# Kernel optimization log

Measured on AMD Instinct MI355X. Metric: run time of the kernel, lower is better.

The kernel has to match this reference:

```python
import jax, jax.numpy as jnp
import numpy as np

N, E, B = 30000, 480000, 64
F_IN, HID, ED = 128, 64, 32
NEG, EPS = 0.2, 1e-5


def _add_self_loops(edge_index, edge_attr):
    # PyG add_self_loops with fill_value='mean': self-loop edge_attr of node i
    # is the mean of edge_attr over edges whose destination is i.
    src, dst = edge_index[0], edge_index[1]
    cnt = jax.ops.segment_sum(jnp.ones((edge_attr.shape[0],), edge_attr.dtype), dst, num_segments=N)
    mean = jax.ops.segment_sum(edge_attr, dst, num_segments=N) / jnp.maximum(cnt, 1.0)[:, None]
    loop = jnp.arange(N)
    return jnp.concatenate([src, loop]), jnp.concatenate([dst, loop]), jnp.concatenate([edge_attr, mean], axis=0)


def _gat_conv(x, src, dst, ea, W, We, a_s, a_d, a_e, bias, H, Fo):
    xs = (x @ W).reshape(-1, H, Fo)              # [N, H, Fo]
    al_src = (xs * a_s).sum(-1)                  # [N, H]
    al_dst = (xs * a_d).sum(-1)                  # [N, H]
    ef = (ea @ We).reshape(-1, H, Fo)            # [Et, H, Fo]
    alpha = al_src[src] + al_dst[dst] + (ef * a_e).sum(-1)   # [Et, H]
    alpha = jax.nn.leaky_relu(alpha, NEG)
    # softmax over incoming edges of each destination node (segment softmax)
    m = jax.ops.segment_max(alpha, dst, num_segments=N)
    ex = jnp.exp(alpha - m[dst])
    s = jax.ops.segment_sum(ex, dst, num_segments=N)
    w = ex / s[dst]                              # [Et, H]
    out = jax.ops.segment_sum(xs[src] * w[:, :, None], dst, num_segments=N)
    return out.reshape(-1, H * Fo) + bias


def _bn(x, g, b):
    # BatchNorm1d in training mode: biased batch statistics over nodes
    mu = x.mean(0)
    var = x.var(0)
    return (x - mu) * jax.lax.rsqrt(var + EPS) * g + b


def _pool(x, batch, Wg, bg):
    # GlobalAttention: softmax(gate_nn(x)) per graph, weighted sum of x
    gate = (x @ Wg + bg)[:, 0]                   # [N]
    m = jax.ops.segment_max(gate, batch, num_segments=B)
    e = jnp.exp(gate - m[batch])
    s = jax.ops.segment_sum(e, batch, num_segments=B)
    w = e / s[batch]
    return jax.ops.segment_sum(x * w[:, None], batch, num_segments=B)   # [B, HID]


def setup_inputs():
    k = jax.random.split(jax.random.key(0), 16)
    g = lambda i, shape, fan: jax.random.normal(k[i], shape, jnp.float32) / np.sqrt(fan)
    return {
        "x": jax.random.normal(k[0], (N, F_IN), jnp.float32),
        "edge_attr": jax.random.normal(k[1], (E, ED), jnp.float32),
        "edge_index": jax.random.randint(k[2], (2, E), 0, N),
        "batch": jnp.sort(jax.random.randint(k[3], (N,), 0, B)),
        "W1": g(4, (F_IN, 4 * HID), F_IN),
        "We1": g(5, (ED, 4 * HID), ED),
        "att_src1": g(6, (4, HID), HID),
        "att_dst1": g(7, (4, HID), HID),
        "att_edge1": g(8, (4, HID), HID),
        "bias1": jnp.zeros((4 * HID,), jnp.float32),
        "g1": jnp.ones((4 * HID,), jnp.float32),
        "b1": jnp.zeros((4 * HID,), jnp.float32),
        "W2": g(9, (4 * HID, HID), 4 * HID),
        "We2": g(10, (ED, HID), ED),
        "att_src2": g(11, (1, HID), HID),
        "att_dst2": g(12, (1, HID), HID),
        "att_edge2": g(13, (1, HID), HID),
        "bias2": jnp.zeros((HID,), jnp.float32),
        "g2": jnp.ones((HID,), jnp.float32),
        "b2": jnp.zeros((HID,), jnp.float32),
        "Wg": g(14, (HID, 1), HID),
        "bg": jnp.zeros((1,), jnp.float32),
    }


def reference(x, edge_attr, edge_index, batch, W1, We1, att_src1, att_dst1, att_edge1, bias1, g1, b1, W2, We2, att_src2, att_dst2, att_edge2, bias2, g2, b2, Wg, bg):
    src, dst, ea = _add_self_loops(edge_index, edge_attr)
    h = jax.nn.relu(_bn(_gat_conv(x, src, dst, ea, W1, We1, att_src1, att_dst1, att_edge1, bias1, 4, HID), g1, b1))
    h = jax.nn.relu(_bn(_gat_conv(h, src, dst, ea, W2, We2, att_src2, att_dst2, att_edge2, bias2, 1, HID), g2, b2))
    return _pool(h, batch, Wg, bg)
```

## Files before the change

kernel.cpp:

```cpp
#include <hip/hip_runtime.h>
#include <math.h>

#define NN 30000
#define EE 480000
#define BB 64

typedef __bf16 b16x8 __attribute__((ext_vector_type(8)));
typedef float  f32x4 __attribute__((ext_vector_type(4)));
typedef unsigned short u16x8 __attribute__((ext_vector_type(8)));

__device__ __forceinline__ float wsum64(float v){
  #pragma unroll
  for (int m = 32; m >= 1; m >>= 1) v += __shfl_xor(v, m, 64);
  return v;
}
__device__ __forceinline__ float wmax64(float v){
  #pragma unroll
  for (int m = 32; m >= 1; m >>= 1) v = fmaxf(v, __shfl_xor(v, m, 64));
  return v;
}
__device__ __forceinline__ float wsum16(float v){
  #pragma unroll
  for (int m = 1; m < 16; m <<= 1) v += __shfl_xor(v, m, 64);
  return v;
}
__device__ __forceinline__ unsigned short f2b(float f){
  union { float f; unsigned u; } v; v.f = f;
  unsigned r = v.u + 0x7fffu + ((v.u >> 16) & 1u);
  return (unsigned short)(r >> 16);
}
__device__ __forceinline__ float b2f(unsigned short u){
  union { unsigned u; float f; } v; v.u = ((unsigned)u) << 16;
  return v.f;
}

__global__ void hist_kernel(const int* __restrict__ dst, int* __restrict__ deg){
  int e = blockIdx.x*256 + threadIdx.x;
  if (e < EE) atomicAdd(&deg[dst[e]], 1);
}

__global__ __launch_bounds__(256) void scan_kernel(const int* __restrict__ deg, int* __restrict__ rowptr){
  __shared__ int s[256];
  __shared__ int wred[4];
  const int b = blockIdx.x, tid = threadIdx.x;
  const int base = b*256;
  int part = 0;
  for (int idx = tid; idx < base; idx += 256) part += deg[idx];
  #pragma unroll
  for (int m = 32; m >= 1; m >>= 1) part += __shfl_xor(part, m, 64);
  if ((tid & 63) == 0) wred[tid >> 6] = part;
  __syncthreads();
  int offset = wred[0] + wred[1] + wred[2] + wred[3];
  int n = base + tid;
  int d = (n < NN) ? deg[n] : 0;
  s[tid] = d;
  __syncthreads();
  for (int off = 1; off < 256; off <<= 1){
    int v = (tid >= off) ? s[tid - off] : 0;
    __syncthreads();
    s[tid] += v;
    __syncthreads();
  }
  if (n < NN) rowptr[n] = offset + s[tid] - d;
  if (b == 0 && tid == 0) rowptr[NN] = EE;
}

__global__ void prep_kernel(const float* __restrict__ W1, const float* __restrict__ W2,
                            const float* __restrict__ We1, const float* __restrict__ ae1,
                            const float* __restrict__ We2, const float* __restrict__ ae2,
                            unsigned short* __restrict__ W1t, unsigned short* __restrict__ W2t,
                            float* __restrict__ wae){
  int t = threadIdx.x, b = blockIdx.x;
  if (b < 128){
    W1t[t*128 + b] = f2b(W1[b*256 + t]);
  } else if (b < 384){
    int k = b - 128;
    if (t < 64) W2t[t*256 + k] = f2b(W2[k*64 + t]);
  } else {
    if (t < 128){
      int h = t >> 5, k = t & 31;
      float s = 0.f;
      for (int f = 0; f < 64; f++) s += We1[k*256 + h*64 + f] * ae1[h*64 + f];
      wae[h*32 + k] = s;
    } else if (t < 160){
      int k = t - 128;
      float s = 0.f;
      for (int f = 0; f < 64; f++) s += We2[k*64 + f] * ae2[f];
      wae[128 + k] = s;
    }
  }
}

__global__ __launch_bounds__(256) void edot_scatter_kernel(const float* __restrict__ ea,
    const float* __restrict__ wae, const int* __restrict__ src, const int* __restrict__ dst,
    const int* __restrict__ rowptr, int* __restrict__ cursor, float* __restrict__ rec){
  __shared__ float s_w[160];
  if (threadIdx.x < 160) s_w[threadIdx.x] = wae[threadIdx.x];
  __syncthreads();
  const int lane = threadIdx.x & 63;
  const int il = lane & 7;
  const int e = blockIdx.x*32 + (threadIdx.x >> 3);
  if (e >= EE) return;
  float4 v = *(const float4*)(ea + (size_t)e*32 + il*4);
  float dots[5];
  #pragma unroll
  for (int h = 0; h < 5; h++){
    float4 w = *(const float4*)&s_w[h*32 + il*4];
    dots[h] = v.x*w.x + v.y*w.y + v.z*w.z + v.w*w.w;
  }
  #pragma unroll
  for (int m = 1; m < 8; m <<= 1)
    #pragma unroll
    for (int h = 0; h < 5; h++) dots[h] += __shfl_xor(dots[h], m, 64);
  int slot = 0;
  if (il == 0){
    int dd = dst[e];
    slot = rowptr[dd] + atomicAdd(&cursor[dd], 1);
  }
  slot = __shfl(slot, lane & ~7, 64);
  if (il == 0){
    float4 lo; lo.x = dots[0]; lo.y = dots[1]; lo.z = dots[2]; lo.w = dots[3];
    *(float4*)(rec + (size_t)slot*8) = lo;
  } else if (il == 1){
    float4 hi; hi.x = dots[4]; hi.y = __int_as_float(src[e]); hi.z = 0.f; hi.w = 0.f;
    *(float4*)(rec + (size_t)slot*8 + 4) = hi;
  }
}

__global__ __launch_bounds__(256) void gemm1_mfma(const float* __restrict__ x,
    const unsigned short* __restrict__ Bt, const float* __restrict__ a_s, const float* __restrict__ a_d,
    unsigned short* __restrict__ out, float* __restrict__ alsrc, float* __restrict__ aldst){
  __shared__ unsigned short As[128*136];
  __shared__ unsigned short Bs[64*136];
  const int tid = threadIdx.x;
  const int w = tid >> 6, lane = tid & 63;
  const int c = lane & 15, gq = lane >> 4;
  const int m0 = blockIdx.x * 128;
  #pragma unroll
  for (int q = 0; q < 16; q++){
    int ch = tid*16 + q;
    int r = ch >> 5, off = (ch & 31)*4;
    int grow = m0 + r;
    ushort4 o;
    if (grow < NN){
      float4 v = *(const float4*)(x + (size_t)grow*128 + off);
      o.x = f2b(v.x); o.y = f2b(v.y); o.z = f2b(v.z); o.w = f2b(v.w);
    } else o = make_ushort4(0,0,0,0);
    *(ushort4*)&As[r*136 + off] = o;
  }
  #pragma unroll
  for (int q = 0; q < 4; q++){
    int ch = tid*4 + q;
    int n = ch >> 4, off = (ch & 15)*8;
    *(ulonglong2*)&Bs[n*136 + off] = *(const ulonglong2*)(Bt + (size_t)n*128 + off);
  }
  __syncthreads();
  for (int head = 0; head < 4; head++){
    f32x4 acc[2][4];
    #pragma unroll
    for (int mt = 0; mt < 2; mt++)
      #pragma unroll
      for (int nt = 0; nt < 4; nt++) acc[mt][nt] = (f32x4){0.f,0.f,0.f,0.f};
    #pragma unroll
    for (int k0 = 0; k0 < 128; k0 += 32){
      b16x8 afr[2], bfr[4];
      #pragma unroll
      for (int mt = 0; mt < 2; mt++)
        afr[mt] = *(const b16x8*)&As[(w*32 + mt*16 + c)*136 + k0 + gq*8];
      #pragma unroll
      for (int nt = 0; nt < 4; nt++)
        bfr[nt] = *(const b16x8*)&Bs[(nt*16 + c)*136 + k0 + gq*8];
      #pragma unroll
      for (int mt = 0; mt < 2; mt++)
        #pragma unroll
        for (int nt = 0; nt < 4; nt++)
          acc[mt][nt] = __builtin_amdgcn_mfma_f32_16x16x32_bf16(afr[mt], bfr[nt], acc[mt][nt], 0, 0, 0);
    }
    __syncthreads();
    if (head < 3){
      #pragma unroll
      for (int q = 0; q < 4; q++){
        int ch = tid*4 + q;
        int n = ch >> 4, off = (ch & 15)*8;
        *(ulonglong2*)&Bs[n*136 + off] = *(const ulonglong2*)(Bt + (size_t)((head+1)*64 + n)*128 + off);
      }
    }
    float asv[4], adv[4];
    #pragma unroll
    for (int nt = 0; nt < 4; nt++){
      asv[nt] = a_s[head*64 + nt*16 + c];
      adv[nt] = a_d[head*64 + nt*16 + c];
    }
    #pragma unroll
    for (int mt = 0; mt < 2; mt++){
      int base_row = m0 + w*32 + mt*16 + gq*4;
      #pragma unroll
      for (int r = 0; r < 4; r++){
        int row = base_row + r;
        float ps = 0.f, pd = 0.f;
        #pragma unroll
        for (int nt = 0; nt < 4; nt++){
          ps += acc[mt][nt][r] * asv[nt];
          pd += acc[mt][nt][r] * adv[nt];
        }
        ps = wsum16(ps); pd = wsum16(pd);
        if (row < NN){
          if (c == 0){
            alsrc[(size_t)row*4 + head] = ps;
            aldst[(size_t)row*4 + head] = pd;
          }
          #pragma unroll
          for (int nt = 0; nt < 4; nt++)
            out[(size_t)row*256 + head*64 + nt*16 + c] = f2b(acc[mt][nt][r]);
        }
      }
    }
    if (head < 3) __syncthreads();
  }
}

__global__ __launch_bounds__(256) void gemm2_mfma(const unsigned short* __restrict__ Ab,
    const unsigned short* __restrict__ Bt,
    const float* __restrict__ cs, const float* __restrict__ csq,
    const float* __restrict__ g, const float* __restrict__ b,
    const float* __restrict__ a_s, const float* __restrict__ a_d,
    unsigned short* __restrict__ out, float* __restrict__ alsrc, float* __restrict__ aldst){
  __shared__ unsigned short As[128*136];
  __shared__ unsigned short Bs[64*136];
  __shared__ float s_scale[256], s_shift[256];
  const int tid = threadIdx.x;
  const int w = tid >> 6, lane = tid & 63;
  const int c = lane & 15, gq = lane >> 4;
  const int m0 = blockIdx.x * 128;
  if (tid < 256){
    float mu  = cs[tid]  * (1.f/NN);
    float var = csq[tid] * (1.f/NN) - mu*mu;
    float rs  = rsqrtf(var + 1e-5f);
    float sc  = rs * g[tid];
    s_scale[tid] = sc;
    s_shift[tid] = b[tid] - mu*sc;
  }
  __syncthreads();
  f32x4 acc[2][4];
  #pragma unroll
  for (int mt = 0; mt < 2; mt++)
    #pragma unroll
    for (int nt = 0; nt < 4; nt++) acc[mt][nt] = (f32x4){0.f,0.f,0.f,0.f};
  for (int kp = 0; kp < 256; kp += 128){
    #pragma unroll
    for (int q = 0; q < 16; q++){
      int ch = tid*16 + q;
      int r = ch >> 5, off = (ch & 31)*4;
      int grow = m0 + r;
      ushort4 o;
      if (grow < NN){
        ushort4 v = *(const ushort4*)(Ab + (size_t)grow*256 + kp + off);
        float4 sc = *(const float4*)&s_scale[kp + off];
        float4 sh = *(const float4*)&s_shift[kp + off];
        o.x = f2b(fmaxf(fmaf(b2f(v.x), sc.x, sh.x), 0.f));
        o.y = f2b(fmaxf(fmaf(b2f(v.y), sc.y, sh.y), 0.f));
        o.z = f2b(fmaxf(fmaf(b2f(v.z), sc.z, sh.z), 0.f));
        o.w = f2b(fmaxf(fmaf(b2f(v.w), sc.w, sh.w), 0.f));
      } else o = make_ushort4(0,0,0,0);
      *(ushort4*)&As[r*136 + off] = o;
    }
    #pragma unroll
    for (int q = 0; q < 4; q++){
      int ch = tid*4 + q;
      int n = ch >> 4, off = (ch & 15)*8;
      *(ulonglong2*)&Bs[n*136 + off] = *(const ulonglong2*)(Bt + (size_t)n*256 + kp + off);
    }
    __syncthreads();
    #pragma unroll
    for (int k0 = 0; k0 < 128; k0 += 32){
      b16x8 afr[2], bfr[4];
      #pragma unroll
      for (int mt = 0; mt < 2; mt++)
        afr[mt] = *(const b16x8*)&As[(w*32 + mt*16 + c)*136 + k0 + gq*8];
      #pragma unroll
      for (int nt = 0; nt < 4; nt++)
        bfr[nt] = *(const b16x8*)&Bs[(nt*16 + c)*136 + k0 + gq*8];
      #pragma unroll
      for (int mt = 0; mt < 2; mt++)
        #pragma unroll
        for (int nt = 0; nt < 4; nt++)
          acc[mt][nt] = __builtin_amdgcn_mfma_f32_16x16x32_bf16(afr[mt], bfr[nt], acc[mt][nt], 0, 0, 0);
    }
    __syncthreads();
  }
  float asv[4], adv[4];
  #pragma unroll
  for (int nt = 0; nt < 4; nt++){
    asv[nt] = a_s[nt*16 + c];
    adv[nt] = a_d[nt*16 + c];
  }
  #pragma unroll
  for (int mt = 0; mt < 2; mt++){
    int base_row = m0 + w*32 + mt*16 + gq*4;
    #pragma unroll
    for (int r = 0; r < 4; r++){
      int row = base_row + r;
      float ps = 0.f, pd = 0.f;
      #pragma unroll
      for (int nt = 0; nt < 4; nt++){
        ps += acc[mt][nt][r] * asv[nt];
        pd += acc[mt][nt][r] * adv[nt];
      }
      ps = wsum16(ps); pd = wsum16(pd);
      if (row < NN){
        if (c == 0){
          alsrc[row] = ps;
          aldst[row] = pd;
        }
        #pragma unroll
        for (int nt = 0; nt < 4; nt++)
          out[(size_t)row*64 + nt*16 + c] = f2b(acc[mt][nt][r]);
      }
    }
  }
}

template<int H>
__global__ __launch_bounds__(256) void agg_kernel(const int* __restrict__ rowptr,
    const float* __restrict__ rec,
    const float* __restrict__ al_src, const float* __restrict__ al_dst,
    const unsigned short* __restrict__ xsb, const float* __restrict__ bias,
    unsigned short* __restrict__ outb, float* __restrict__ outf){
  constexpr int CH = 128;
  __shared__ float s_e_all[4][CH*H];
  __shared__ int   s_src_all[4][CH];
  const int wid  = threadIdx.x >> 6;
  const int lane = threadIdx.x & 63;
  const int i = blockIdx.x*4 + wid;
  float* s_e  = s_e_all[wid];
  int*   s_src = s_src_all[wid];
  const int r0 = rowptr[i];
  const int d  = rowptr[i+1] - r0;
  float ad[H], asi[H];
  #pragma unroll
  for (int h = 0; h < H; h++){ ad[h] = al_dst[(size_t)i*H+h]; asi[h] = al_src[(size_t)i*H+h]; }
  float sesum[H], m[H];
  #pragma unroll
  for (int h = 0; h < H; h++){ sesum[h] = 0.f; m[h] = -1e30f; }
  for (int t = lane; t < d; t += 64){
    const float* rp = rec + (size_t)(r0 + t)*8;
    float al[H];
    int sn;
    if constexpr (H == 4){
      float4 ev = *(const float4*)rp;
      float2 hi = *(const float2*)(rp + 4);
      sn = __float_as_int(hi.y);
      float4 av = *(const float4*)(al_src + (size_t)sn*4);
      al[0]=av.x+ad[0]+ev.x; al[1]=av.y+ad[1]+ev.y; al[2]=av.z+ad[2]+ev.z; al[3]=av.w+ad[3]+ev.w;
      sesum[0]+=ev.x; sesum[1]+=ev.y; sesum[2]+=ev.z; sesum[3]+=ev.w;
    } else {
      float2 hi = *(const float2*)(rp + 4);
      sn = __float_as_int(hi.y);
      al[0] = al_src[sn] + ad[0] + hi.x;
      sesum[0] += hi.x;
    }
    if (t < CH) s_src[t] = sn;
    #pragma unroll
    for (int h = 0; h < H; h++){
      float a = al[h]; a = a > 0.f ? a : 0.2f*a;
      if (t < CH) s_e[t*H+h] = a;
      m[h] = fmaxf(m[h], a);
    }
  }
  float invd = (d > 0) ? 1.f/(float)d : 0.f;
  float sa[H];
  #pragma unroll
  for (int h = 0; h < H; h++){
    sesum[h] = wsum64(sesum[h]);
    m[h] = wmax64(m[h]);
    float a = asi[h] + ad[h] + sesum[h]*invd;
    sa[h] = a > 0.f ? a : 0.2f*a;
    m[h] = fmaxf(m[h], sa[h]);
  }
  float acc8[8];
  #pragma unroll
  for (int j = 0; j < 8; j++) acc8[j] = 0.f;
  float dpart[H];
  #pragma unroll
  for (int h = 0; h < H; h++) dpart[h] = 0.f;
  const int half = lane >> 5, il5 = lane & 31;
  const int grp  = lane >> 3, il3 = lane & 7;
  int c0 = 0;
  while (c0 < d){
    int cl = min(CH, d - c0);
    if (c0 > 0){
      for (int t = lane; t < cl; t += 64){
        const float* rp = rec + (size_t)(r0 + c0 + t)*8;
        if constexpr (H == 4){
          float4 ev = *(const float4*)rp;
          float2 hi = *(const float2*)(rp + 4);
          int sn = __float_as_int(hi.y);
          s_src[t] = sn;
          float4 av = *(const float4*)(al_src + (size_t)sn*4);
          float a0=av.x+ad[0]+ev.x, a1=av.y+ad[1]+ev.y, a2=av.z+ad[2]+ev.z, a3=av.w+ad[3]+ev.w;
          s_e[t*4+0]=a0>0.f?a0:0.2f*a0; s_e[t*4+1]=a1>0.f?a1:0.2f*a1;
          s_e[t*4+2]=a2>0.f?a2:0.2f*a2; s_e[t*4+3]=a3>0.f?a3:0.2f*a3;
        } else {
          float2 hi = *(const float2*)(rp + 4);
          int sn = __float_as_int(hi.y);
          s_src[t] = sn;
          float a = al_src[sn] + ad[0] + hi.x;
          s_e[t] = a > 0.f ? a : 0.2f*a;
        }
      }
    }
    for (int t = lane; t < cl; t += 64){
      #pragma unroll
      for (int h = 0; h < H; h++){
        float e = __expf(s_e[t*H+h] - m[h]);
        s_e[t*H+h] = e;
        dpart[h] += e;
      }
    }
    __builtin_amdgcn_wave_barrier();
    if constexpr (H == 4){
      const int hd = il5 >> 3;
      for (int t = half; t < cl; t += 2){
        int sn = s_src[t];
        float wv = s_e[t*4 + hd];
        u16x8 u = *(const u16x8*)(xsb + (size_t)sn*256 + il5*8);
        #pragma unroll
        for (int j = 0; j < 8; j++) acc8[j] += wv * b2f(u[j]);
      }
    } else {
      for (int t = grp; t < cl; t += 8){
        int sn = s_src[t];
        float wv = s_e[t];
        u16x8 u = *(const u16x8*)(xsb + (size_t)sn*64 + il3*8);
        #pragma unroll
        for (int j = 0; j < 8; j++) acc8[j] += wv * b2f(u[j]);
      }
    }
    __builtin_amdgcn_wave_barrier();
    c0 += CH;
  }
  float es[H];
  #pragma unroll
  for (int h = 0; h < H; h++) es[h] = __expf(sa[h] - m[h]);
  if (lane == 0){
    #pragma unroll
    for (int h = 0; h < H; h++) dpart[h] += es[h];
  }
  if constexpr (H == 4){
    if (half == 0){
      float wv = es[il5 >> 3];
      u16x8 u = *(const u16x8*)(xsb + (size_t)i*256 + il5*8);
      #pragma unroll
      for (int j = 0; j < 8; j++) acc8[j] += wv * b2f(u[j]);
    }
  } else {
    if (grp == 0){
      float wv = es[0];
      u16x8 u = *(const u16x8*)(xsb + (size_t)i*64 + il3*8);
      #pragma unroll
      for (int j = 0; j < 8; j++) acc8[j] += wv * b2f(u[j]);
    }
  }
  float denom[H];
  #pragma unroll
  for (int h = 0; h < H; h++) denom[h] = wsum64(dpart[h]);
  if constexpr (H == 4){
    #pragma unroll
    for (int j = 0; j < 8; j++) acc8[j] += __shfl_xor(acc8[j], 32, 64);
    if (lane < 32){
      float inv = 1.f / denom[il5 >> 3];
      u16x8 o;
      #pragma unroll
      for (int j = 0; j < 8; j++) o[j] = f2b(acc8[j]*inv + bias[il5*8 + j]);
      *(u16x8*)(outb + (size_t)i*256 + il5*8) = o;
    }
  } else {
    #pragma unroll
    for (int j = 0; j < 8; j++){
      acc8[j] += __shfl_xor(acc8[j], 8, 64);
      acc8[j] += __shfl_xor(acc8[j], 16, 64);
      acc8[j] += __shfl_xor(acc8[j], 32, 64);
    }
    if (lane < 8){
      float inv = 1.f / denom[0];
      float4 o0, o1;
      o0.x = acc8[0]*inv + bias[il3*8+0]; o0.y = acc8[1]*inv + bias[il3*8+1];
      o0.z = acc8[2]*inv + bias[il3*8+2]; o0.w = acc8[3]*inv + bias[il3*8+3];
      o1.x = acc8[4]*inv + bias[il3*8+4]; o1.y = acc8[5]*inv + bias[il3*8+5];
      o1.z = acc8[6]*inv + bias[il3*8+6]; o1.w = acc8[7]*inv + bias[il3*8+7];
      *(float4*)(outf + (size_t)i*64 + il3*8)     = o0;
      *(float4*)(outf + (size_t)i*64 + il3*8 + 4) = o1;
    }
  }
}

__global__ __launch_bounds__(256) void bn_stats_b16_kernel(const unsigned short* __restrict__ h,
    float* __restrict__ cs, float* __restrict__ csq){
  __shared__ float s_red[4][256], q_red[4][256];
  const int tid = threadIdx.x;
  const int wv = tid >> 6, lane = tid & 63;
  const int rg = lane >> 5, cg = lane & 31;
  float s8[8], q8[8];
  #pragma unroll
  for (int j = 0; j < 8; j++){ s8[j] = 0.f; q8[j] = 0.f; }
  for (int chunk = blockIdx.x; chunk < 3750; chunk += 256){
    int r = chunk*8 + wv*2 + rg;
    u16x8 u = *(const u16x8*)(h + (size_t)r*256 + cg*8);
    #pragma unroll
    for (int j = 0; j < 8; j++){
      float v = b2f(u[j]);
      s8[j] += v; q8[j] += v*v;
    }
  }
  #pragma unroll
  for (int j = 0; j < 8; j++){
    s8[j] += __shfl_xor(s8[j], 32, 64);
    q8[j] += __shfl_xor(q8[j], 32, 64);
  }
  if (lane < 32){
    #pragma unroll
    for (int j = 0; j < 8; j++){
      s_red[wv][cg*8 + j] = s8[j];
      q_red[wv][cg*8 + j] = q8[j];
    }
  }
  __syncthreads();
  if (tid < 256){
    float ts = s_red[0][tid] + s_red[1][tid] + s_red[2][tid] + s_red[3][tid];
    float tq = q_red[0][tid] + q_red[1][tid] + q_red[2][tid] + q_red[3][tid];
    atomicAdd(&cs[tid], ts);
    atomicAdd(&csq[tid], tq);
  }
}

__global__ __launch_bounds__(256) void bn_stats_f32_kernel(const float* __restrict__ h,
    float* __restrict__ cs, float* __restrict__ csq){
  int col = threadIdx.x & 63;
  int ro  = threadIdx.x >> 6;
  float s = 0.f, s2 = 0.f;
  for (int r = blockIdx.x*4 + ro; r < NN; r += 1024){
    float v = h[(size_t)r*64 + col];
    s += v; s2 += v*v;
  }
  atomicAdd(&cs[col], s);
  atomicAdd(&csq[col], s2);
}

__global__ __launch_bounds__(256) void gate_kernel(const float* __restrict__ h,
    const float* __restrict__ cs, const float* __restrict__ csq,
    const float* __restrict__ g2, const float* __restrict__ b2,
    const float* __restrict__ Wg, const float* __restrict__ bg,
    float* __restrict__ hn, float* __restrict__ gate){
  int wid = threadIdx.x >> 6, lane = threadIdx.x & 63;
  int n = blockIdx.x*4 + wid;
  float mu  = cs[lane]  * (1.f/NN);
  float var = csq[lane] * (1.f/NN) - mu*mu;
  float rs  = rsqrtf(var + 1e-5f);
  float sc  = rs * g2[lane];
  float sh  = b2[lane] - mu*sc;
  float v = h[(size_t)n*64 + lane];
  float xx = fmaxf(fmaf(v, sc, sh), 0.f);
  hn[(size_t)n*64 + lane] = xx;
  float p = wsum64(xx * Wg[lane]);
  if (lane == 0) gate[n] = p + bg[0];
}

__global__ __launch_bounds__(256) void pool_kernel(const int* __restrict__ batch,
    const float* __restrict__ gate, const float* __restrict__ hn, float* __restrict__ out){
  __shared__ float red[256];
  __shared__ float a_red[4][64], w_red[4];
  __shared__ int seb[2];
  int b = blockIdx.x, tid = threadIdx.x;
  int wv = tid >> 6, lane = tid & 63;
  if (tid < 2){
    int target = b + tid;
    int lo = 0, hi = NN;
    while (lo < hi){ int mid = (lo+hi) >> 1; if (batch[mid] < target) lo = mid+1; else hi = mid; }
    seb[tid] = lo;
  }
  __syncthreads();
  int s = seb[0], e = seb[1];
  if (e <= s){ if (tid < 64) out[b*64 + tid] = 0.f; return; }
  float mloc = -1e30f;
  for (int n = s + tid; n < e; n += 256) mloc = fmaxf(mloc, gate[n]);
  mloc = wmax64(mloc);
  if (lane == 0) red[wv] = mloc;
  __syncthreads();
  float m = fmaxf(fmaxf(red[0], red[1]), fmaxf(red[2], red[3]));
  int rgrp = tid >> 4, cq = tid & 15;
  f32x4 acc = (f32x4){0.f,0.f,0.f,0.f};
  float wp = 0.f;
  for (int n = s + rgrp; n < e; n += 16){
    float wgt = __expf(gate[n] - m);
    float4 v = *(const float4*)(hn + (size_t)n*64 + cq*4);
    acc[0] += wgt*v.x; acc[1] += wgt*v.y; acc[2] += wgt*v.z; acc[3] += wgt*v.w;
    if (cq == 0) wp += wgt;
  }
  #pragma unroll
  for (int j = 0; j < 4; j++){
    acc[j] += __shfl_xor(acc[j], 16, 64);
    acc[j] += __shfl_xor(acc[j], 32, 64);
  }
  wp += __shfl_xor(wp, 16, 64);
  wp += __shfl_xor(wp, 32, 64);
  if (lane < 16){
    #pragma unroll
    for (int j = 0; j < 4; j++) a_red[wv][lane*4 + j] = acc[j];
  }
  if (lane == 0) w_red[wv] = wp;
  __syncthreads();
  if (tid < 64){
    float tot = a_red[0][tid] + a_red[1][tid] + a_red[2][tid] + a_red[3][tid];
    float wsm = w_red[0] + w_red[1] + w_red[2] + w_red[3];
    out[b*64 + tid] = tot / wsm;
  }
}

extern "C" void kernel_launch(void* const* d_in, const int* in_sizes, int n_in,
                              void* d_out, int out_size, void* d_ws, size_t ws_size,
                              hipStream_t stream){
  const float* x     = (const float*)d_in[0];
  const float* ea    = (const float*)d_in[1];
  const int*   ei    = (const int*)d_in[2];
  const int*   batch = (const int*)d_in[3];
  const float* W1    = (const float*)d_in[4];
  const float* We1   = (const float*)d_in[5];
  const float* as1   = (const float*)d_in[6];
  const float* ad1   = (const float*)d_in[7];
  const float* ae1   = (const float*)d_in[8];
  const float* bias1 = (const float*)d_in[9];
  const float* g1    = (const float*)d_in[10];
  const float* b1    = (const float*)d_in[11];
  const float* W2    = (const float*)d_in[12];
  const float* We2   = (const float*)d_in[13];
  const float* as2   = (const float*)d_in[14];
  const float* ad2   = (const float*)d_in[15];
  const float* ae2   = (const float*)d_in[16];
  const float* bias2 = (const float*)d_in[17];
  const float* g2    = (const float*)d_in[18];
  const float* b2    = (const float*)d_in[19];
  const float* Wg    = (const float*)d_in[20];
  const float* bg    = (const float*)d_in[21];
  const int* srcI = ei;
  const int* dstI = ei + EE;

  char* ws = (char*)d_ws;
  int*   deg    = (int*)(ws + 0);
  int*   cursor = (int*)(ws + 120064);
  float* stats  = (float*)(ws + 240128);
  int*   rowptr = (int*)(ws + 244224);
  float* wae    = (float*)(ws + 364288);
  unsigned short* W1t = (unsigned short*)(ws + 365056);
  unsigned short* W2t = (unsigned short*)(ws + 430592);
  float* alsrc  = (float*)(ws + 463360);
  float* aldst  = (float*)(ws + 943360);
  float* gateb  = (float*)(ws + 1423360);
  float* rec    = (float*)(ws + 1543424);
  unsigned short* xs1b = (unsigned short*)(ws + 16903424);
  unsigned short* h1b  = (unsigned short*)(ws + 32263424);
  unsigned short* xs2b = (unsigned short*)(ws + 47623424);
  float* h2     = (float*)(ws + 51463424);
  float* hn     = (float*)(ws + 59143424);

  (void)hipMemsetAsync(ws, 0, 244224, stream);

  hist_kernel<<<1875, 256, 0, stream>>>(dstI, deg);
  scan_kernel<<<118, 256, 0, stream>>>(deg, rowptr);
  prep_kernel<<<385, 256, 0, stream>>>(W1, W2, We1, ae1, We2, ae2, W1t, W2t, wae);
  edot_scatter_kernel<<<15000, 256, 0, stream>>>(ea, wae, srcI, dstI, rowptr, cursor, rec);

  gemm1_mfma<<<235, 256, 0, stream>>>(x, W1t, as1, ad1, xs1b, alsrc, aldst);
  agg_kernel<4><<<7500, 256, 0, stream>>>(rowptr, rec, alsrc, aldst, xs1b, bias1, h1b, nullptr);
  bn_stats_b16_kernel<<<256, 256, 0, stream>>>(h1b, stats + 0, stats + 256);

  gemm2_mfma<<<235, 256, 0, stream>>>(h1b, W2t, stats + 0, stats + 256, g1, b1,
                                      as2, ad2, xs2b, alsrc, aldst);
  agg_kernel<1><<<7500, 256, 0, stream>>>(rowptr, rec, alsrc, aldst, xs2b, bias2, nullptr, h2);
  bn_stats_f32_kernel<<<256, 256, 0, stream>>>(h2, stats + 512, stats + 576);

  gate_kernel<<<7500, 256, 0, stream>>>(h2, stats + 512, stats + 576, g2, b2, Wg, bg, hn, gateb);
  pool_kernel<<<64, 256, 0, stream>>>(batch, gateb, hn, (float*)d_out);
}
```

Measured before the change: 364.4 us.

## Add compact layer-2 edge records, split gemm1 over heads, fuse BN into pool

The edge kernel now also writes a compact 8-byte record (layer-2 edge logit plus source index) per edge, so the single-head aggregation reads half-size records instead of strided 32-byte ones. It also moves the atomic slot reservation and src load earlier to overlap them with the dot products. gemm1 is split across a second grid dimension so each block handles two heads, doubling the block count for better occupancy. The normalized h buffer is dropped and pool applies BN+ReLU on the fly, removing a write and read of an N×64 float array at the cost of extra per-element math and an extra record write in the edge pass.

```diff
diff --git a/kernel.cpp b/kernel.cpp
--- a/kernel.cpp
+++ b/kernel.cpp
@@ -91,9 +91,10 @@
   }
 }
 
-__global__ __launch_bounds__(256) void edot_scatter_kernel(const float* __restrict__ ea,
+__global__ __launch_bounds__(256) void edge_kernel(const float* __restrict__ ea,
     const float* __restrict__ wae, const int* __restrict__ src, const int* __restrict__ dst,
-    const int* __restrict__ rowptr, int* __restrict__ cursor, float* __restrict__ rec){
+    const int* __restrict__ rowptr, int* __restrict__ cursor,
+    float* __restrict__ rec, float2* __restrict__ rec8){
   __shared__ float s_w[160];
   if (threadIdx.x < 160) s_w[threadIdx.x] = wae[threadIdx.x];
   __syncthreads();
@@ -101,6 +102,12 @@
   const int il = lane & 7;
   const int e = blockIdx.x*32 + (threadIdx.x >> 3);
   if (e >= EE) return;
+  int slot = 0, sv = 0;
+  if (il == 0){
+    int dd = dst[e];
+    slot = rowptr[dd] + atomicAdd(&cursor[dd], 1);
+    sv = src[e];
+  }
   float4 v = *(const float4*)(ea + (size_t)e*32 + il*4);
   float dots[5];
   #pragma unroll
@@ -112,18 +119,17 @@
   for (int m = 1; m < 8; m <<= 1)
     #pragma unroll
     for (int h = 0; h < 5; h++) dots[h] += __shfl_xor(dots[h], m, 64);
-  int slot = 0;
-  if (il == 0){
-    int dd = dst[e];
-    slot = rowptr[dd] + atomicAdd(&cursor[dd], 1);
-  }
   slot = __shfl(slot, lane & ~7, 64);
+  sv   = __shfl(sv,   lane & ~7, 64);
   if (il == 0){
     float4 lo; lo.x = dots[0]; lo.y = dots[1]; lo.z = dots[2]; lo.w = dots[3];
     *(float4*)(rec + (size_t)slot*8) = lo;
   } else if (il == 1){
-    float4 hi; hi.x = dots[4]; hi.y = __int_as_float(src[e]); hi.z = 0.f; hi.w = 0.f;
+    float4 hi; hi.x = dots[4]; hi.y = __int_as_float(sv); hi.z = 0.f; hi.w = 0.f;
     *(float4*)(rec + (size_t)slot*8 + 4) = hi;
+  } else if (il == 2){
+    float2 r8; r8.x = dots[4]; r8.y = __int_as_float(sv);
+    rec8[slot] = r8;
   }
 }
 
@@ -136,6 +142,7 @@
   const int w = tid >> 6, lane = tid & 63;
   const int c = lane & 15, gq = lane >> 4;
   const int m0 = blockIdx.x * 128;
+  const int h0 = blockIdx.y * 2;
   #pragma unroll
   for (int q = 0; q < 16; q++){
     int ch = tid*16 + q;
@@ -152,10 +159,11 @@
   for (int q = 0; q < 4; q++){
     int ch = tid*4 + q;
     int n = ch >> 4, off = (ch & 15)*8;
-    *(ulonglong2*)&Bs[n*136 + off] = *(const ulonglong2*)(Bt + (size_t)n*128 + off);
-  }
-  __syncthreads();
-  for (int head = 0; head < 4; head++){
+    *(ulonglong2*)&Bs[n*136 + off] = *(const ulonglong2*)(Bt + (size_t)(h0*64 + n)*128 + off);
+  }
+  __syncthreads();
+  for (int hi = 0; hi < 2; hi++){
+    const int head = h0 + hi;
     f32x4 acc[2][4];
     #pragma unroll
     for (int mt = 0; mt < 2; mt++)
@@ -177,12 +185,12 @@
           acc[mt][nt] = __builtin_amdgcn_mfma_f32_16x16x32_bf16(afr[mt], bfr[nt], acc[mt][nt], 0, 0, 0);
     }
     __syncthreads();
-    if (head < 3){
+    if (hi == 0){
       #pragma unroll
       for (int q = 0; q < 4; q++){
         int ch = tid*4 + q;
         int n = ch >> 4, off = (ch & 15)*8;
-        *(ulonglong2*)&Bs[n*136 + off] = *(const ulonglong2*)(Bt + (size_t)((head+1)*64 + n)*128 + off);
+        *(ulonglong2*)&Bs[n*136 + off] = *(const ulonglong2*)(Bt + (size_t)((h0+1)*64 + n)*128 + off);
       }
     }
     float asv[4], adv[4];
@@ -215,7 +223,7 @@
         }
       }
     }
-    if (head < 3) __syncthreads();
+    if (hi == 0) __syncthreads();
   }
 }
 
@@ -232,7 +240,7 @@
   const int w = tid >> 6, lane = tid & 63;
   const int c = lane & 15, gq = lane >> 4;
   const int m0 = blockIdx.x * 128;
-  if (tid < 256){
+  {
     float mu  = cs[tid]  * (1.f/NN);
     float var = csq[tid] * (1.f/NN) - mu*mu;
     float rs  = rsqrtf(var + 1e-5f);
@@ -343,10 +351,10 @@
   #pragma unroll
   for (int h = 0; h < H; h++){ sesum[h] = 0.f; m[h] = -1e30f; }
   for (int t = lane; t < d; t += 64){
-    const float* rp = rec + (size_t)(r0 + t)*8;
     float al[H];
     int sn;
     if constexpr (H == 4){
+      const float* rp = rec + (size_t)(r0 + t)*8;
       float4 ev = *(const float4*)rp;
       float2 hi = *(const float2*)(rp + 4);
       sn = __float_as_int(hi.y);
@@ -354,7 +362,7 @@
       al[0]=av.x+ad[0]+ev.x; al[1]=av.y+ad[1]+ev.y; al[2]=av.z+ad[2]+ev.z; al[3]=av.w+ad[3]+ev.w;
       sesum[0]+=ev.x; sesum[1]+=ev.y; sesum[2]+=ev.z; sesum[3]+=ev.w;
     } else {
-      float2 hi = *(const float2*)(rp + 4);
+      float2 hi = ((const float2*)rec)[r0 + t];
       sn = __float_as_int(hi.y);
       al[0] = al_src[sn] + ad[0] + hi.x;
       sesum[0] += hi.x;
@@ -390,8 +398,8 @@
     int cl = min(CH, d - c0);
     if (c0 > 0){
       for (int t = lane; t < cl; t += 64){
-        const float* rp = rec + (size_t)(r0 + c0 + t)*8;
         if constexpr (H == 4){
+          const float* rp = rec + (size_t)(r0 + c0 + t)*8;
           float4 ev = *(const float4*)rp;
           float2 hi = *(const float2*)(rp + 4);
           int sn = __float_as_int(hi.y);
@@ -401,7 +409,7 @@
           s_e[t*4+0]=a0>0.f?a0:0.2f*a0; s_e[t*4+1]=a1>0.f?a1:0.2f*a1;
           s_e[t*4+2]=a2>0.f?a2:0.2f*a2; s_e[t*4+3]=a3>0.f?a3:0.2f*a3;
         } else {
-          float2 hi = *(const float2*)(rp + 4);
+          float2 hi = ((const float2*)rec)[r0 + c0 + t];
           int sn = __float_as_int(hi.y);
           s_src[t] = sn;
           float a = al_src[sn] + ad[0] + hi.x;
@@ -550,7 +558,7 @@
     const float* __restrict__ cs, const float* __restrict__ csq,
     const float* __restrict__ g2, const float* __restrict__ b2,
     const float* __restrict__ Wg, const float* __restrict__ bg,
-    float* __restrict__ hn, float* __restrict__ gate){
+    float* __restrict__ gate){
   int wid = threadIdx.x >> 6, lane = threadIdx.x & 63;
   int n = blockIdx.x*4 + wid;
   float mu  = cs[lane]  * (1.f/NN);
@@ -560,13 +568,15 @@
   float sh  = b2[lane] - mu*sc;
   float v = h[(size_t)n*64 + lane];
   float xx = fmaxf(fmaf(v, sc, sh), 0.f);
-  hn[(size_t)n*64 + lane] = xx;
   float p = wsum64(xx * Wg[lane]);
   if (lane == 0) gate[n] = p + bg[0];
 }
 
 __global__ __launch_bounds__(256) void pool_kernel(const int* __restrict__ batch,
-    const float* __restrict__ gate, const float* __restrict__ hn, float* __restrict__ out){
+    const float* __restrict__ gate, const float* __restrict__ h2,
+    const float* __restrict__ cs, const float* __restrict__ csq,
+    const float* __restrict__ g2, const float* __restrict__ b2,
+    float* __restrict__ out){
   __shared__ float red[256];
   __shared__ float a_red[4][64], w_red[4];
   __shared__ int seb[2];
@@ -588,12 +598,29 @@
   __syncthreads();
   float m = fmaxf(fmaxf(red[0], red[1]), fmaxf(red[2], red[3]));
   int rgrp = tid >> 4, cq = tid & 15;
+  float4 csv = *(const float4*)(cs + cq*4);
+  float4 cqv = *(const float4*)(csq + cq*4);
+  float4 gv  = *(const float4*)(g2 + cq*4);
+  float4 bv  = *(const float4*)(b2 + cq*4);
+  float4 scv, shv;
+  {
+    float mu0 = csv.x*(1.f/NN), mu1 = csv.y*(1.f/NN), mu2 = csv.z*(1.f/NN), mu3 = csv.w*(1.f/NN);
+    scv.x = rsqrtf(cqv.x*(1.f/NN) - mu0*mu0 + 1e-5f) * gv.x;
+    scv.y = rsqrtf(cqv.y*(1.f/NN) - mu1*mu1 + 1e-5f) * gv.y;
+    scv.z = rsqrtf(cqv.z*(1.f/NN) - mu2*mu2 + 1e-5f) * gv.z;
+    scv.w = rsqrtf(cqv.w*(1.f/NN) - mu3*mu3 + 1e-5f) * gv.w;
+    shv.x = bv.x - mu0*scv.x; shv.y = bv.y - mu1*scv.y;
+    shv.z = bv.z - mu2*scv.z; shv.w = bv.w - mu3*scv.w;
+  }
   f32x4 acc = (f32x4){0.f,0.f,0.f,0.f};
   float wp = 0.f;
   for (int n = s + rgrp; n < e; n += 16){
     float wgt = __expf(gate[n] - m);
-    float4 v = *(const float4*)(hn + (size_t)n*64 + cq*4);
-    acc[0] += wgt*v.x; acc[1] += wgt*v.y; acc[2] += wgt*v.z; acc[3] += wgt*v.w;
+    float4 v = *(const float4*)(h2 + (size_t)n*64 + cq*4);
+    acc[0] += wgt*fmaxf(fmaf(v.x, scv.x, shv.x), 0.f);
+    acc[1] += wgt*fmaxf(fmaf(v.y, scv.y, shv.y), 0.f);
+    acc[2] += wgt*fmaxf(fmaf(v.z, scv.z, shv.z), 0.f);
+    acc[3] += wgt*fmaxf(fmaf(v.w, scv.w, shv.w), 0.f);
     if (cq == 0) wp += wgt;
   }
   #pragma unroll
@@ -660,24 +687,24 @@
   unsigned short* h1b  = (unsigned short*)(ws + 32263424);
   unsigned short* xs2b = (unsigned short*)(ws + 47623424);
   float* h2     = (float*)(ws + 51463424);
-  float* hn     = (float*)(ws + 59143424);
+  float2* rec8  = (float2*)(ws + 59143424);
 
   (void)hipMemsetAsync(ws, 0, 244224, stream);
 
   hist_kernel<<<1875, 256, 0, stream>>>(dstI, deg);
   scan_kernel<<<118, 256, 0, stream>>>(deg, rowptr);
   prep_kernel<<<385, 256, 0, stream>>>(W1, W2, We1, ae1, We2, ae2, W1t, W2t, wae);
-  edot_scatter_kernel<<<15000, 256, 0, stream>>>(ea, wae, srcI, dstI, rowptr, cursor, rec);
-
-  gemm1_mfma<<<235, 256, 0, stream>>>(x, W1t, as1, ad1, xs1b, alsrc, aldst);
+  edge_kernel<<<15000, 256, 0, stream>>>(ea, wae, srcI, dstI, rowptr, cursor, rec, rec8);
+
+  gemm1_mfma<<<dim3(235, 2), 256, 0, stream>>>(x, W1t, as1, ad1, xs1b, alsrc, aldst);
   agg_kernel<4><<<7500, 256, 0, stream>>>(rowptr, rec, alsrc, aldst, xs1b, bias1, h1b, nullptr);
   bn_stats_b16_kernel<<<256, 256, 0, stream>>>(h1b, stats + 0, stats + 256);
 
   gemm2_mfma<<<235, 256, 0, stream>>>(h1b, W2t, stats + 0, stats + 256, g1, b1,
                                       as2, ad2, xs2b, alsrc, aldst);
-  agg_kernel<1><<<7500, 256, 0, stream>>>(rowptr, rec, alsrc, aldst, xs2b, bias2, nullptr, h2);
+  agg_kernel<1><<<7500, 256, 0, stream>>>(rowptr, (const float*)rec8, alsrc, aldst, xs2b, bias2, nullptr, h2);
   bn_stats_f32_kernel<<<256, 256, 0, stream>>>(h2, stats + 512, stats + 576);
 
-  gate_kernel<<<7500, 256, 0, stream>>>(h2, stats + 512, stats + 576, g2, b2, Wg, bg, hn, gateb);
-  pool_kernel<<<64, 256, 0, stream>>>(batch, gateb, hn, (float*)d_out);
-}
+  gate_kernel<<<7500, 256, 0, stream>>>(h2, stats + 512, stats + 576, g2, b2, Wg, bg, gateb);
+  pool_kernel<<<64, 256, 0, stream>>>(batch, gateb, h2, stats + 512, stats + 576, g2, b2, (float*)d_out);
+}
```

Result: slower. 373.4 us (+2.5%).
